# Performance work log

Hardware: AMD Instinct MI355X
Metric: run time of the kernel (lower is better)

Reference implementation:

```python
import jax, jax.numpy as jnp
import numpy as np
import math

B, S, D, H = 2, 2048, 1024, 16
DQ = D // H  # d_qkv = 64


def setup_inputs() -> dict:
    key = jax.random.key(0)
    k1, k2, k3, k4 = jax.random.split(key, 4)
    return {
        "Q": jax.random.normal(k1, (B, S, D), dtype=jnp.float32),
        "K": jax.random.normal(k2, (B, S, D), dtype=jnp.float32),
        "V": jax.random.normal(k3, (B, S, D), dtype=jnp.float32),
        "Wo_w": jax.random.normal(k4, (D, D), dtype=jnp.float32) * 0.02,
        "Wo_b": jnp.zeros((D,), dtype=jnp.float32),
        "mask": 1,
    }


def reference(Q, K, V, Wo_w, Wo_b, mask):
    # Note: original module defines Wq/Wk/Wv but never applies them in forward.
    q = Q.reshape(B, S, H, DQ)
    k = K.reshape(B, S, H, DQ)
    v = V.reshape(B, S, H, DQ)
    # raw QK^T scores: [B, H, S, S]
    scores = jnp.einsum("bqhd,bkhd->bhqk", q, k)
    if mask:
        # torch.triu_indices(S, S) default offset=0 -> mask where key >= query
        # (diagonal included). Fill applied BEFORE the sqrt(d) scaling, as in source.
        tri = jnp.arange(S)[:, None] <= jnp.arange(S)[None, :]  # [S, S]
        scores = jnp.where(tri, jnp.float32(-1e9), scores)
    scale = scores / math.sqrt(DQ)
    attn = jax.nn.softmax(scale, axis=-1)
    ctx = jnp.einsum("bhqk,bkhd->bqhd", attn, v).reshape(B, S, D)
    return ctx @ Wo_w.T + Wo_b
```

## Files before the change

kernel.cpp:

```cpp
#include <hip/hip_runtime.h>
#include <hip/hip_bf16.h>
#include <stdint.h>

#define B_  2
#define S_  2048
#define D_  1024
#define H_  16
#define DQ_ 64
#define QT_ (S_/64)

#define C1_ 0.18033688011112042f

typedef float f32x4  __attribute__((ext_vector_type(4)));
typedef float f32x16 __attribute__((ext_vector_type(16)));
typedef short bf16x8 __attribute__((ext_vector_type(8)));

__device__ __forceinline__ unsigned short f2bf(float f) {
    uint32_t u = __float_as_uint(f);
    u += 0x7fffu + ((u >> 16) & 1u);
    return (unsigned short)(u >> 16);
}
__device__ __forceinline__ float bf2f(unsigned short u) {
    return __uint_as_float(((uint32_t)u) << 16);
}
__device__ __forceinline__ bf16x8 packbf8s(float4 a, float4 b, float sc) {
    bf16x8 r;
    r[0]=(short)f2bf(a.x*sc); r[1]=(short)f2bf(a.y*sc);
    r[2]=(short)f2bf(a.z*sc); r[3]=(short)f2bf(a.w*sc);
    r[4]=(short)f2bf(b.x*sc); r[5]=(short)f2bf(b.y*sc);
    r[6]=(short)f2bf(b.z*sc); r[7]=(short)f2bf(b.w*sc);
    return r;
}
__device__ __forceinline__ float fast_exp2(float x) {
#if __has_builtin(__builtin_amdgcn_exp2f)
    return __builtin_amdgcn_exp2f(x);
#else
    float r; asm("v_exp_f32 %0, %1" : "=v"(r) : "v"(x)); return r;
#endif
}
__device__ __forceinline__ uint32_t cvt_pk_bf16(float lo, float hi) {
    uint32_t r;
    asm("v_cvt_pk_bf16_f32 %0, %1, %2" : "=v"(r) : "v"(lo), "v"(hi));
    return r;
}
__device__ __forceinline__ void permlane32_swap(uint32_t &a, uint32_t &b) {
    asm volatile("v_permlane32_swap_b32 %0, %1" : "+v"(a), "+v"(b));
}

__global__ __launch_bounds__(256) void prep_kernel(
    const float* __restrict__ K, const float* __restrict__ V,
    const float* __restrict__ W,
    unsigned short* __restrict__ Kf, unsigned short* __restrict__ Vf,
    unsigned short* __restrict__ Wb, float* __restrict__ Pv)
{
    __shared__ unsigned short Ls[64][72];
    __shared__ float Pp[8][64];
    const int blk = blockIdx.x, tid = threadIdx.x;

    if (blk < 2048) {
        const bool isV = blk < 1024;
        const int gb = isV ? blk : (blk - 1024);
        const int g = gb >> 5, j = gb & 31;
        const int b = g >> 4, h = g & 15;
        const float* src0 = (isV ? V : K) + ((size_t)(b*S_ + j*64))*D_ + h*64;

        {
            int row = tid >> 2, col0 = (tid & 3) * 16;
            const float* src = src0 + (size_t)row*D_ + col0;
            float4 f0 = ((const float4*)src)[0];
            float4 f1 = ((const float4*)src)[1];
            float4 f2 = ((const float4*)src)[2];
            float4 f3 = ((const float4*)src)[3];
            unsigned short* d = &Ls[row][col0];
            d[0]=f2bf(f0.x); d[1]=f2bf(f0.y); d[2]=f2bf(f0.z); d[3]=f2bf(f0.w);
            d[4]=f2bf(f1.x); d[5]=f2bf(f1.y); d[6]=f2bf(f1.z); d[7]=f2bf(f1.w);
            d[8]=f2bf(f2.x); d[9]=f2bf(f2.y); d[10]=f2bf(f2.z); d[11]=f2bf(f2.w);
            d[12]=f2bf(f3.x); d[13]=f2bf(f3.y); d[14]=f2bf(f3.z); d[15]=f2bf(f3.w);
        }
        __syncthreads();

        if (isV) {
            #pragma unroll
            for (int ps = 0; ps < 2; ++ps) {
                const int slot = tid + ps*256;
                const int fb = slot >> 6, l = slot & 63;
                const int s = fb >> 1, kk = fb & 1;
                const int hi = l >> 5, l31 = l & 31;
                const int dcol = kk*32 + l31;
                unsigned short us[8];
                float p = 0.f;
                #pragma unroll
                for (int r = 0; r < 8; ++r) {
                    unsigned short u = Ls[s*16 + hi*8 + r][dcol];
                    us[r] = u;
                    p += bf2f(u);
                }
                *(uint4*)(Vf + ((size_t)gb*8 + fb)*512 + (size_t)l*8) = *(uint4*)us;
                Pp[s*2 + hi][dcol] = p;
            }
            __syncthreads();
            if (tid < 64) {
                float t = 0.f;
                #pragma unroll
                for (int i = 0; i < 8; ++i) t += Pp[i][tid];
                Pv[((size_t)g*64 + tid)*32 + j] = t;
            }
        } else {
            #pragma unroll
            for (int ps = 0; ps < 2; ++ps) {
                const int slot = tid + ps*256;
                const int fb = slot >> 6, l = slot & 63;
                const int wk = fb >> 2, s = fb & 3;
                const int hi = l >> 5, l31 = l & 31;
                uint4 val = *(const uint4*)&Ls[wk*32 + l31][s*16 + hi*8];
                *(uint4*)(Kf + ((size_t)gb*8 + fb)*512 + (size_t)l*8) = val;
            }
        }
    } else {
        int i = (blk - 2048)*256 + tid;
        float4 f = ((const float4*)W)[i];
        ushort4 o;
        o.x = f2bf(f.x); o.y = f2bf(f.y); o.z = f2bf(f.z); o.w = f2bf(f.w);
        ((ushort4*)Wb)[i] = o;
    }
}

__global__ __launch_bounds__(256, 2) void attn_kernel(
    const float* __restrict__ Q,
    const unsigned short* __restrict__ Kf,
    const unsigned short* __restrict__ Vf,
    const float* __restrict__ Pv,
    unsigned short* __restrict__ ctx,
    const int* __restrict__ maskp)
{
    __shared__ float Osum[2][32][68];
    __shared__ float Lsum[2][32];

    const int bid = blockIdx.x;
    const int g = bid & 31;
    const int p = bid >> 5;
    const int qt = (p < 8) ? p : (p < 16) ? 23 - p : (p < 24) ? p : 55 - p;
    const int h = g & 15, b = g >> 4;
    const int tid  = threadIdx.x;
    const int wave = tid >> 6, lane = tid & 63;
    const int wq = wave >> 1, wk = wave & 1;
    const int hi = lane >> 5, l31 = lane & 31;
    const int maskv = maskp[0];

    if (maskv && qt == 0 && tid < 64) {
        const float* pv = Pv + ((size_t)g*64 + tid)*32;
        float s = 0.f;
        #pragma unroll
        for (int i = 0; i < 32; ++i) s += pv[i];
        ctx[(size_t)b*S_*D_ + h*64 + tid] = f2bf(s * (1.0f/S_));
    }

    const unsigned short* kfb =
        Kf + ((size_t)g*32*8 + wk*4)*512 + (size_t)lane*8;
    const unsigned short* vfb =
        Vf + ((size_t)g*32*8 + wk*4)*512 + (size_t)lane*8;

    int njw = maskv ? (qt + 1) : QT_;
    if (maskv && wq == 0 && wk == 1) njw = qt;

    const int q0 = qt*64 + wq*32 + l31;
    const float* qrow = Q + ((size_t)(b*S_ + q0))*D_ + h*64;
    bf16x8 qf[4];
    #pragma unroll
    for (int s = 0; s < 4; ++s) {
        float4 f0 = ((const float4*)(qrow + s*16 + hi*8))[0];
        float4 f1 = ((const float4*)(qrow + s*16 + hi*8))[1];
        qf[s] = packbf8s(f0, f1, C1_);
    }

    f32x16 o[2] = {};
    float lsum = 0.f;

    bf16x8 kc[4], vc[4], kn[4], vn[4];
    const unsigned short* kfj = kfb;
    const unsigned short* vfj = vfb;
    if (njw > 0) {
        #pragma unroll
        for (int s = 0; s < 4; ++s) {
            kc[s] = *(const bf16x8*)(kfj + s*512);
            vc[s] = *(const bf16x8*)(vfj + s*512);
        }
    }

    for (int j = 0; j < njw; ++j) {
        if (j + 1 < njw) {
            const unsigned short* kp = kfj + 8*512;
            const unsigned short* vp = vfj + 8*512;
            #pragma unroll
            for (int s = 0; s < 4; ++s) {
                kn[s] = *(const bf16x8*)(kp + s*512);
                vn[s] = *(const bf16x8*)(vp + s*512);
            }
        }

        f32x16 st = {};
        #pragma unroll
        for (int s = 0; s < 4; ++s)
            st = __builtin_amdgcn_mfma_f32_32x32x16_bf16(kc[s], qf[s], st, 0,0,0);

        const bool diag = maskv && (j == qt) && (wk == wq);
        float e[16];
        #pragma unroll
        for (int r = 0; r < 16; ++r) {
            float ev = fast_exp2(st[r]);
            if (diag) {
                int kr = (r&3) + 8*(r>>2) + 4*hi;
                ev = (kr >= l31) ? 0.f : ev;
            }
            e[r] = ev;
            lsum += ev;
        }

        uint32_t p01 = cvt_pk_bf16(e[0], e[1]);
        uint32_t p23 = cvt_pk_bf16(e[2], e[3]);
        uint32_t p45 = cvt_pk_bf16(e[4], e[5]);
        uint32_t p67 = cvt_pk_bf16(e[6], e[7]);
        permlane32_swap(p01, p45);
        permlane32_swap(p23, p67);
        uint32_t r01 = cvt_pk_bf16(e[8],  e[9]);
        uint32_t r23 = cvt_pk_bf16(e[10], e[11]);
        uint32_t r45 = cvt_pk_bf16(e[12], e[13]);
        uint32_t r67 = cvt_pk_bf16(e[14], e[15]);
        permlane32_swap(r01, r45);
        permlane32_swap(r23, r67);
        union { uint32_t u[4]; bf16x8 v; } pa0, pa1;
        pa0.u[0]=p01; pa0.u[1]=p23; pa0.u[2]=p45; pa0.u[3]=p67;
        pa1.u[0]=r01; pa1.u[1]=r23; pa1.u[2]=r45; pa1.u[3]=r67;

        o[0] = __builtin_amdgcn_mfma_f32_32x32x16_bf16(pa0.v, vc[0], o[0], 0,0,0);
        o[1] = __builtin_amdgcn_mfma_f32_32x32x16_bf16(pa0.v, vc[1], o[1], 0,0,0);
        o[0] = __builtin_amdgcn_mfma_f32_32x32x16_bf16(pa1.v, vc[2], o[0], 0,0,0);
        o[1] = __builtin_amdgcn_mfma_f32_32x32x16_bf16(pa1.v, vc[3], o[1], 0,0,0);

        #pragma unroll
        for (int s = 0; s < 4; ++s) { kc[s] = kn[s]; vc[s] = vn[s]; }
        kfj += 8*512; vfj += 8*512;
    }

    lsum += __shfl_xor(lsum, 32);

    if (wk == 1) {
        #pragma unroll
        for (int r = 0; r < 16; ++r) {
            int qr = (r&3) + 8*(r>>2) + 4*hi;
            Osum[wq][qr][l31]      = o[0][r];
            Osum[wq][qr][32 + l31] = o[1][r];
        }
        if (hi == 0) Lsum[wq][l31] = lsum;
    }
    __syncthreads();
    if (wk == 0) {
        float inv = 1.0f / (lsum + Lsum[wq][l31]);
        #pragma unroll
        for (int r = 0; r < 16; ++r) {
            int qr = (r&3) + 8*(r>>2) + 4*hi;
            float o0v = o[0][r] + Osum[wq][qr][l31];
            float o1v = o[1][r] + Osum[wq][qr][32 + l31];
            float invr = __shfl(inv, qr);
            int q = qt*64 + wq*32 + qr;
            if (!(maskv && q == 0)) {
                size_t base = ((size_t)(b*S_ + q))*D_ + h*64;
                ctx[base + l31]      = f2bf(o0v * invr);
                ctx[base + 32 + l31] = f2bf(o1v * invr);
            }
        }
    }
}

__global__ __launch_bounds__(256, 2) void proj_kernel(
    const unsigned short* __restrict__ A,
    const unsigned short* __restrict__ Bw,
    const float* __restrict__ bias,
    float* __restrict__ out)
{
    __shared__ unsigned short As[2][64][72];
    __shared__ unsigned short Bs[2][128][72];
    const int nt0 = blockIdx.x;
    const int mt0 = blockIdx.y;
    const int tid  = threadIdx.x;
    const int wave = tid >> 6, lane = tid & 63;
    const int quad = lane >> 4, ln = lane & 15;

    const int arow = tid >> 2, acol = (tid & 3)*16;
    const int brow = tid >> 1, bcol = (tid & 1)*32;
    const unsigned short* aptr = A  + ((size_t)(mt0*64  + arow)*1024 + acol);
    const unsigned short* bptr = Bw + ((size_t)(nt0*128 + brow)*1024 + bcol);

    uint4 a0 = ((const uint4*)aptr)[0], a1 = ((const uint4*)aptr)[1];
    uint4 b0 = ((const uint4*)bptr)[0], b1 = ((const uint4*)bptr)[1],
          b2 = ((const uint4*)bptr)[2], b3 = ((const uint4*)bptr)[3];

    f32x4 acc[4][2] = {};

    for (int kt = 0; kt < 16; ++kt) {
        const int cur = kt & 1;
        *((uint4*)&As[cur][arow][acol])    = a0;
        *((uint4*)&As[cur][arow][acol+8])  = a1;
        *((uint4*)&Bs[cur][brow][bcol])    = b0;
        *((uint4*)&Bs[cur][brow][bcol+8])  = b1;
        *((uint4*)&Bs[cur][brow][bcol+16]) = b2;
        *((uint4*)&Bs[cur][brow][bcol+24]) = b3;
        uint4 na0, na1, nb0, nb1, nb2, nb3;
        if (kt < 15) {
            const unsigned short* ap = aptr + (kt+1)*64;
            const unsigned short* bp = bptr + (kt+1)*64;
            na0 = ((const uint4*)ap)[0]; na1 = ((const uint4*)ap)[1];
            nb0 = ((const uint4*)bp)[0]; nb1 = ((const uint4*)bp)[1];
            nb2 = ((const uint4*)bp)[2]; nb3 = ((const uint4*)bp)[3];
        }
        __syncthreads();
        #pragma unroll
        for (int ks = 0; ks < 2; ++ks) {
            bf16x8 am[4], bn[2];
            #pragma unroll
            for (int i = 0; i < 4; ++i)
                am[i] = *(const bf16x8*)&As[cur][i*16 + ln][ks*32 + quad*8];
            #pragma unroll
            for (int i = 0; i < 2; ++i)
                bn[i] = *(const bf16x8*)&Bs[cur][wave*32 + i*16 + ln][ks*32 + quad*8];
            #pragma unroll
            for (int mi = 0; mi < 4; ++mi)
                #pragma unroll
                for (int ni = 0; ni < 2; ++ni)
                    acc[mi][ni] = __builtin_amdgcn_mfma_f32_16x16x32_bf16(
                        am[mi], bn[ni], acc[mi][ni], 0,0,0);
        }
        a0 = na0; a1 = na1;
        b0 = nb0; b1 = nb1; b2 = nb2; b3 = nb3;
    }

    #pragma unroll
    for (int mi = 0; mi < 4; ++mi)
        #pragma unroll
        for (int ni = 0; ni < 2; ++ni) {
            int row = mt0*64 + mi*16 + quad*4;
            int col = nt0*128 + wave*32 + ni*16 + ln;
            float bv = bias[col];
            #pragma unroll
            for (int r = 0; r < 4; ++r)
                out[(size_t)(row + r)*1024 + col] = acc[mi][ni][r] + bv;
        }
}

extern "C" void kernel_launch(void* const* d_in, const int* in_sizes, int n_in,
                              void* d_out, int out_size, void* d_ws, size_t ws_size,
                              hipStream_t stream)
{
    const float* Q   = (const float*)d_in[0];
    const float* K   = (const float*)d_in[1];
    const float* V   = (const float*)d_in[2];
    const float* Wo  = (const float*)d_in[3];
    const float* Wb  = (const float*)d_in[4];
    const int* maskp = (const int*)d_in[5];
    float* out = (float*)d_out;

    unsigned short* Kf   = (unsigned short*)d_ws;
    unsigned short* Vf   = Kf  + (size_t)B_*S_*D_;
    unsigned short* Wob  = Vf  + (size_t)B_*S_*D_;
    unsigned short* ctxb = Wob + (size_t)D_*D_;
    float* Pv = (float*)(ctxb + (size_t)B_*S_*D_);

    prep_kernel<<<3072, 256, 0, stream>>>(K, V, Wo, Kf, Vf, Wob, Pv);
    attn_kernel<<<1024, 256, 0, stream>>>(Q, Kf, Vf, Pv, ctxb, maskp);
    proj_kernel<<<dim3(8, 64), 256, 0, stream>>>(ctxb, Wob, Wb, out);
}
```

Baseline: 148.5 us.

## Stage Q through shared memory and double-buffer K/V loads two tiles ahead

Q is now loaded cooperatively once per block into shared memory as scaled bf16, so the wave pairs no longer each read the same fp32 Q rows from global memory, and each wave then reads its fragments from LDS. The K/V loop is unrolled by two with ping-pong register buffers, and the next K and V loads are issued right after the MFMAs that consume the current ones, keeping loads two tiles ahead. s_setprio is raised around the MFMA groups, and the diagonal mask check is hoisted out of the exp loop. The shared Q buffer shares storage with the reduction scratch through a union, which adds two extra barriers.

```diff
diff --git a/kernel.cpp b/kernel.cpp
--- a/kernel.cpp
+++ b/kernel.cpp
@@ -22,14 +22,6 @@
 }
 __device__ __forceinline__ float bf2f(unsigned short u) {
     return __uint_as_float(((uint32_t)u) << 16);
-}
-__device__ __forceinline__ bf16x8 packbf8s(float4 a, float4 b, float sc) {
-    bf16x8 r;
-    r[0]=(short)f2bf(a.x*sc); r[1]=(short)f2bf(a.y*sc);
-    r[2]=(short)f2bf(a.z*sc); r[3]=(short)f2bf(a.w*sc);
-    r[4]=(short)f2bf(b.x*sc); r[5]=(short)f2bf(b.y*sc);
-    r[6]=(short)f2bf(b.z*sc); r[7]=(short)f2bf(b.w*sc);
-    return r;
 }
 __device__ __forceinline__ float fast_exp2(float x) {
 #if __has_builtin(__builtin_amdgcn_exp2f)
@@ -133,8 +125,10 @@
     unsigned short* __restrict__ ctx,
     const int* __restrict__ maskp)
 {
-    __shared__ float Osum[2][32][68];
-    __shared__ float Lsum[2][32];
+    __shared__ union {
+        unsigned short qs[64][72];
+        struct { float osum[2][32][68]; float lsum[2][32]; } red;
+    } sm;
 
     const int bid = blockIdx.x;
     const int g = bid & 31;
@@ -155,6 +149,26 @@
         ctx[(size_t)b*S_*D_ + h*64 + tid] = f2bf(s * (1.0f/S_));
     }
 
+    {
+        const int row = tid >> 2, col0 = (tid & 3) * 16;
+        const float* src = Q + ((size_t)(b*S_ + qt*64 + row))*D_ + h*64 + col0;
+        float4 f0 = ((const float4*)src)[0];
+        float4 f1 = ((const float4*)src)[1];
+        float4 f2 = ((const float4*)src)[2];
+        float4 f3 = ((const float4*)src)[3];
+        unsigned short* d = &sm.qs[row][col0];
+        d[0]=f2bf(f0.x*C1_); d[1]=f2bf(f0.y*C1_); d[2]=f2bf(f0.z*C1_); d[3]=f2bf(f0.w*C1_);
+        d[4]=f2bf(f1.x*C1_); d[5]=f2bf(f1.y*C1_); d[6]=f2bf(f1.z*C1_); d[7]=f2bf(f1.w*C1_);
+        d[8]=f2bf(f2.x*C1_); d[9]=f2bf(f2.y*C1_); d[10]=f2bf(f2.z*C1_); d[11]=f2bf(f2.w*C1_);
+        d[12]=f2bf(f3.x*C1_); d[13]=f2bf(f3.y*C1_); d[14]=f2bf(f3.z*C1_); d[15]=f2bf(f3.w*C1_);
+    }
+    __syncthreads();
+    bf16x8 qf[4];
+    #pragma unroll
+    for (int s = 0; s < 4; ++s)
+        qf[s] = *(const bf16x8*)&sm.qs[wq*32 + l31][s*16 + hi*8];
+    __syncthreads();
+
     const unsigned short* kfb =
         Kf + ((size_t)g*32*8 + wk*4)*512 + (size_t)lane*8;
     const unsigned short* vfb =
@@ -163,84 +177,86 @@
     int njw = maskv ? (qt + 1) : QT_;
     if (maskv && wq == 0 && wk == 1) njw = qt;
 
-    const int q0 = qt*64 + wq*32 + l31;
-    const float* qrow = Q + ((size_t)(b*S_ + q0))*D_ + h*64;
-    bf16x8 qf[4];
-    #pragma unroll
-    for (int s = 0; s < 4; ++s) {
-        float4 f0 = ((const float4*)(qrow + s*16 + hi*8))[0];
-        float4 f1 = ((const float4*)(qrow + s*16 + hi*8))[1];
-        qf[s] = packbf8s(f0, f1, C1_);
-    }
-
     f32x16 o[2] = {};
     float lsum = 0.f;
 
-    bf16x8 kc[4], vc[4], kn[4], vn[4];
-    const unsigned short* kfj = kfb;
-    const unsigned short* vfj = vfb;
+    bf16x8 ka[4], va[4], kb[4], vb[4];
     if (njw > 0) {
         #pragma unroll
         for (int s = 0; s < 4; ++s) {
-            kc[s] = *(const bf16x8*)(kfj + s*512);
-            vc[s] = *(const bf16x8*)(vfj + s*512);
-        }
-    }
-
-    for (int j = 0; j < njw; ++j) {
-        if (j + 1 < njw) {
-            const unsigned short* kp = kfj + 8*512;
-            const unsigned short* vp = vfj + 8*512;
-            #pragma unroll
-            for (int s = 0; s < 4; ++s) {
-                kn[s] = *(const bf16x8*)(kp + s*512);
-                vn[s] = *(const bf16x8*)(vp + s*512);
-            }
-        }
-
-        f32x16 st = {};
-        #pragma unroll
-        for (int s = 0; s < 4; ++s)
-            st = __builtin_amdgcn_mfma_f32_32x32x16_bf16(kc[s], qf[s], st, 0,0,0);
-
-        const bool diag = maskv && (j == qt) && (wk == wq);
-        float e[16];
-        #pragma unroll
-        for (int r = 0; r < 16; ++r) {
-            float ev = fast_exp2(st[r]);
-            if (diag) {
-                int kr = (r&3) + 8*(r>>2) + 4*hi;
-                ev = (kr >= l31) ? 0.f : ev;
-            }
-            e[r] = ev;
-            lsum += ev;
-        }
-
-        uint32_t p01 = cvt_pk_bf16(e[0], e[1]);
-        uint32_t p23 = cvt_pk_bf16(e[2], e[3]);
-        uint32_t p45 = cvt_pk_bf16(e[4], e[5]);
-        uint32_t p67 = cvt_pk_bf16(e[6], e[7]);
-        permlane32_swap(p01, p45);
-        permlane32_swap(p23, p67);
-        uint32_t r01 = cvt_pk_bf16(e[8],  e[9]);
-        uint32_t r23 = cvt_pk_bf16(e[10], e[11]);
-        uint32_t r45 = cvt_pk_bf16(e[12], e[13]);
-        uint32_t r67 = cvt_pk_bf16(e[14], e[15]);
-        permlane32_swap(r01, r45);
-        permlane32_swap(r23, r67);
-        union { uint32_t u[4]; bf16x8 v; } pa0, pa1;
-        pa0.u[0]=p01; pa0.u[1]=p23; pa0.u[2]=p45; pa0.u[3]=p67;
-        pa1.u[0]=r01; pa1.u[1]=r23; pa1.u[2]=r45; pa1.u[3]=r67;
-
-        o[0] = __builtin_amdgcn_mfma_f32_32x32x16_bf16(pa0.v, vc[0], o[0], 0,0,0);
-        o[1] = __builtin_amdgcn_mfma_f32_32x32x16_bf16(pa0.v, vc[1], o[1], 0,0,0);
-        o[0] = __builtin_amdgcn_mfma_f32_32x32x16_bf16(pa1.v, vc[2], o[0], 0,0,0);
-        o[1] = __builtin_amdgcn_mfma_f32_32x32x16_bf16(pa1.v, vc[3], o[1], 0,0,0);
-
-        #pragma unroll
-        for (int s = 0; s < 4; ++s) { kc[s] = kn[s]; vc[s] = vn[s]; }
-        kfj += 8*512; vfj += 8*512;
-    }
+            ka[s] = *(const bf16x8*)(kfb + s*512);
+            va[s] = *(const bf16x8*)(vfb + s*512);
+        }
+    }
+    if (njw > 1) {
+        #pragma unroll
+        for (int s = 0; s < 4; ++s) {
+            kb[s] = *(const bf16x8*)(kfb + 4096 + s*512);
+            vb[s] = *(const bf16x8*)(vfb + 4096 + s*512);
+        }
+    }
+
+#define AITER(J, KC, VC)                                                      \
+  {                                                                           \
+    f32x16 st = {};                                                           \
+    __builtin_amdgcn_s_setprio(1);                                            \
+    st = __builtin_amdgcn_mfma_f32_32x32x16_bf16(KC[0], qf[0], st, 0,0,0);    \
+    st = __builtin_amdgcn_mfma_f32_32x32x16_bf16(KC[1], qf[1], st, 0,0,0);    \
+    st = __builtin_amdgcn_mfma_f32_32x32x16_bf16(KC[2], qf[2], st, 0,0,0);    \
+    st = __builtin_amdgcn_mfma_f32_32x32x16_bf16(KC[3], qf[3], st, 0,0,0);    \
+    __builtin_amdgcn_s_setprio(0);                                            \
+    if ((J) + 2 < njw) {           \
+      const unsigned short* kp_ = kfb + (size_t)((J)+2)*4096;                 \
+      KC[0] = *(const bf16x8*)(kp_);                                          \
+      KC[1] = *(const bf16x8*)(kp_ + 512);                                    \
+      KC[2] = *(const bf16x8*)(kp_ + 1024);                                   \
+      KC[3] = *(const bf16x8*)(kp_ + 1536);                                   \
+    }                                                                         \
+    float e[16];                                                              \
+    const bool diag_ = maskv && ((J) == qt) && (wk == wq);                    \
+    if (diag_) {                                                              \
+      _Pragma("unroll")                                                       \
+      for (int r = 0; r < 16; ++r) {                                          \
+        int kr_ = (r&3) + 8*(r>>2) + 4*hi;                                    \
+        float ev_ = fast_exp2(st[r]);                                         \
+        e[r] = (kr_ >= l31) ? 0.f : ev_;                                      \
+        lsum += e[r];                                                         \
+      }                                                                       \
+    } else {                                                                  \
+      _Pragma("unroll")                                                       \
+      for (int r = 0; r < 16; ++r) { e[r] = fast_exp2(st[r]); lsum += e[r]; } \
+    }                                                                         \
+    uint32_t p01_ = cvt_pk_bf16(e[0], e[1]),  p23_ = cvt_pk_bf16(e[2], e[3]); \
+    uint32_t p45_ = cvt_pk_bf16(e[4], e[5]),  p67_ = cvt_pk_bf16(e[6], e[7]); \
+    permlane32_swap(p01_, p45_); permlane32_swap(p23_, p67_);                 \
+    uint32_t r01_ = cvt_pk_bf16(e[8], e[9]),  r23_ = cvt_pk_bf16(e[10], e[11]); \
+    uint32_t r45_ = cvt_pk_bf16(e[12], e[13]), r67_ = cvt_pk_bf16(e[14], e[15]); \
+    permlane32_swap(r01_, r45_); permlane32_swap(r23_, r67_);                 \
+    union { uint32_t u[4]; bf16x8 v; } A0_, A1_;                              \
+    A0_.u[0]=p01_; A0_.u[1]=p23_; A0_.u[2]=p45_; A0_.u[3]=p67_;               \
+    A1_.u[0]=r01_; A1_.u[1]=r23_; A1_.u[2]=r45_; A1_.u[3]=r67_;               \
+    __builtin_amdgcn_s_setprio(1);                                            \
+    o[0] = __builtin_amdgcn_mfma_f32_32x32x16_bf16(A0_.v, VC[0], o[0], 0,0,0);\
+    o[1] = __builtin_amdgcn_mfma_f32_32x32x16_bf16(A0_.v, VC[1], o[1], 0,0,0);\
+    o[0] = __builtin_amdgcn_mfma_f32_32x32x16_bf16(A1_.v, VC[2], o[0], 0,0,0);\
+    o[1] = __builtin_amdgcn_mfma_f32_32x32x16_bf16(A1_.v, VC[3], o[1], 0,0,0);\
+    __builtin_amdgcn_s_setprio(0);                                            \
+    if ((J) + 2 < njw) {           \
+      const unsigned short* vp_ = vfb + (size_t)((J)+2)*4096;                 \
+      VC[0] = *(const bf16x8*)(vp_);                                          \
+      VC[1] = *(const bf16x8*)(vp_ + 512);                                    \
+      VC[2] = *(const bf16x8*)(vp_ + 1024);                                   \
+      VC[3] = *(const bf16x8*)(vp_ + 1536);                                   \
+    }                                                                         \
+  }
+
+    int j = 0;
+    for (; j + 1 < njw; j += 2) {
+        AITER(j, ka, va);
+        AITER(j+1, kb, vb);
+    }
+    if (j < njw) AITER(j, ka, va);
+#undef AITER
 
     lsum += __shfl_xor(lsum, 32);
 
@@ -248,19 +264,19 @@
         #pragma unroll
         for (int r = 0; r < 16; ++r) {
             int qr = (r&3) + 8*(r>>2) + 4*hi;
-            Osum[wq][qr][l31]      = o[0][r];
-            Osum[wq][qr][32 + l31] = o[1][r];
-        }
-        if (hi == 0) Lsum[wq][l31] = lsum;
+            sm.red.osum[wq][qr][l31]      = o[0][r];
+            sm.red.osum[wq][qr][32 + l31] = o[1][r];
+        }
+        if (hi == 0) sm.red.lsum[wq][l31] = lsum;
     }
     __syncthreads();
     if (wk == 0) {
-        float inv = 1.0f / (lsum + Lsum[wq][l31]);
+        float inv = 1.0f / (lsum + sm.red.lsum[wq][l31]);
         #pragma unroll
         for (int r = 0; r < 16; ++r) {
             int qr = (r&3) + 8*(r>>2) + 4*hi;
-            float o0v = o[0][r] + Osum[wq][qr][l31];
-            float o1v = o[1][r] + Osum[wq][qr][32 + l31];
+            float o0v = o[0][r] + sm.red.osum[wq][qr][l31];
+            float o1v = o[1][r] + sm.red.osum[wq][qr][32 + l31];
             float invr = __shfl(inv, qr);
             int q = qt*64 + wq*32 + qr;
             if (!(maskv && q == 0)) {
```

Measured after the change: 143.6 us. 1.03x faster.
